# Performance work log

Hardware: AMD Instinct MI355X
Metric: run time of the kernel (lower is better)

## Reference

```python
import jax, jax.numpy as jnp
import numpy as np

N = 262144          # anchors
NUM_CLASSES = 80
DET_DIM = 4 + NUM_CLASSES
TOP_K = 1000
MAX_BOXES = 300
NMS_THRESHOLD = 0.4


def setup_inputs() -> dict:
    key = jax.random.key(0)
    k1, k2, k3, k4, k5 = jax.random.split(key, 5)
    # boxes in (x1, y1, x2, y2) format with x2 > x1, y2 > y1
    xy1 = jax.random.uniform(k1, (1, N, 2), dtype=jnp.float32) * 1000.0
    wh = jax.random.uniform(k2, (1, N, 2), dtype=jnp.float32) * 100.0 + 1.0
    boxes = jnp.concatenate([xy1, xy1 + wh], axis=-1)              # [1, N, 4]
    classification = jax.random.uniform(k3, (1, N, NUM_CLASSES), dtype=jnp.float32)
    detections = jax.random.normal(k4, (1, N, DET_DIM), dtype=jnp.float32)
    return {"boxes": boxes, "classification": classification, "detections": detections}


def _iou_matrix(b):
    # b: [K, 4] in (x1, y1, x2, y2)
    x1, y1, x2, y2 = b[:, 0], b[:, 1], b[:, 2], b[:, 3]
    area = (x2 - x1) * (y2 - y1)
    ix1 = jnp.maximum(x1[:, None], x1[None, :])
    iy1 = jnp.maximum(y1[:, None], y1[None, :])
    ix2 = jnp.minimum(x2[:, None], x2[None, :])
    iy2 = jnp.minimum(y2[:, None], y2[None, :])
    inter = jnp.maximum(ix2 - ix1, 0.0) * jnp.maximum(iy2 - iy1, 0.0)
    union = area[:, None] + area[None, :] - inter
    return inter / jnp.maximum(union, 1e-8)


def _nms(boxes, scores, iou_threshold, max_output_size):
    # Greedy NMS (tf.image.non_max_suppression semantics) on K boxes.
    K = boxes.shape[0]
    order = jnp.argsort(-scores)              # descending score
    iou = _iou_matrix(boxes[order])           # [K, K] in sorted order
    ar = jnp.arange(K)

    def body(suppressed, i):
        active = jnp.logical_not(suppressed[i])
        suppressed = suppressed | (active & (iou[i] > iou_threshold) & (ar > i))
        return suppressed, active

    _, keep = jax.lax.scan(body, jnp.zeros((K,), jnp.bool_), ar)
    # fixed-size selection of kept positions (in score order), padded with K
    sel = jnp.nonzero(keep, size=max_output_size, fill_value=K)[0]
    valid = sel < K
    order_pad = jnp.concatenate([order, jnp.zeros((1,), order.dtype)])
    return order_pad[sel], valid


def reference(boxes, classification, detections):
    b = boxes[0]                               # [N, 4]
    c = classification[0]                      # [N, C]
    d = detections[0]                          # [N, D]
    scores = jnp.max(c, axis=1)                # per-anchor best class score
    scores_k, idx_k = jax.lax.top_k(scores, TOP_K)
    b_k = b[idx_k]                             # [TOP_K, 4]
    d_k = d[idx_k]                             # [TOP_K, D]
    nms_idx, valid = _nms(b_k, scores_k, NMS_THRESHOLD, MAX_BOXES)
    # original returns a ragged [1, n_kept, D]; we return fixed [1, MAX_BOXES, D]
    # with invalid rows zeroed (padding for jit-compatibility)
    out = d_k[nms_idx] * valid[:, None].astype(d_k.dtype)
    return out[None]                           # [1, MAX_BOXES, D]
```

## Files before the change

### kernel.cpp

```cpp
#include <hip/hip_runtime.h>
#include <stdint.h>

#define N_ANCH 262144
#define NUM_CLASSES 80
#define DET_DIM 84
#define TOP_K 1000
#define MAX_BOXES 300
#define NMS_THR 0.4f

#define OFF_KEYS   0u
#define OFF_HIST1  (N_ANCH * 4u)
#define OFF_HIST2  (OFF_HIST1 + 16384u)
#define OFF_HIST3  (OFF_HIST2 + 16384u)
#define OFF_STATE  (OFF_HIST3 + 1024u)
#define OFF_LISTA  (OFF_STATE + 64u)
#define OFF_LISTB  (OFF_LISTA + 4096u)
#define OFF_TOPK   (OFF_LISTB + 16384u)
#define OFF_BOXK   (OFF_TOPK + 4096u)
#define OFF_MASK   (OFF_BOXK + 16384u)
#define OFF_SEL    (OFF_MASK + 131072u)

#define ZERO_WORDS ((16384u + 16384u + 1024u + 64u) / 4u)

__global__ __launch_bounds__(256) void k_init(uint32_t* __restrict__ z) {
    uint32_t tid = blockIdx.x * 256u + threadIdx.x;
    if (tid < ZERO_WORDS) z[tid] = 0u;
}

__global__ __launch_bounds__(256) void k_scores(const float* __restrict__ cls,
                                                uint32_t* __restrict__ keys,
                                                uint32_t* __restrict__ ghist1) {
    __shared__ uint32_t h[4096];
    for (int i = threadIdx.x; i < 4096; i += 256) h[i] = 0u;
    __syncthreads();
    int q = threadIdx.x & 3;
    int stride = gridDim.x * 64;
    for (int a = blockIdx.x * 64 + (threadIdx.x >> 2); a < N_ANCH; a += stride) {
        const float4* p = (const float4*)(cls + (size_t)a * NUM_CLASSES) + q;
        float m = -1.0f;
#pragma unroll
        for (int t = 0; t < 5; ++t) {
            float4 v = p[4 * t];
            m = fmaxf(m, fmaxf(fmaxf(v.x, v.y), fmaxf(v.z, v.w)));
        }
        m = fmaxf(m, __shfl_xor(m, 1));
        m = fmaxf(m, __shfl_xor(m, 2));
        if (q == 0) {
            uint32_t key = __float_as_uint(m);
            keys[a] = key;
            atomicAdd(&h[key >> 20], 1u);
        }
    }
    __syncthreads();
    for (int i = threadIdx.x; i < 4096; i += 256) {
        uint32_t v = h[i];
        if (v) atomicAdd(&ghist1[i], v);
    }
}

__device__ __forceinline__ void wave_scan_hist(const uint32_t* __restrict__ hist,
                                               int nbins, uint32_t k,
                                               uint32_t* __restrict__ out, int lane) {
    int per = nbins >> 6;
    int base = lane * per;
    uint32_t partial = 0;
    for (int b = 0; b < per; ++b) partial += hist[base + b];
    uint32_t si = partial;
#pragma unroll
    for (int off = 1; off < 64; off <<= 1) {
        uint32_t v = __shfl_down(si, off);
        if (lane + off < 64) si += v;
    }
    uint32_t se = si - partial;
    if (se < k && k <= si) {
        uint32_t running = se;
        for (int b = base + per - 1; b >= base; --b) {
            uint32_t hv = hist[b];
            running += hv;
            if (running >= k) {
                out[0] = (uint32_t)b;
                out[1] = k - (running - hv);
                break;
            }
        }
    }
}

__global__ __launch_bounds__(256) void k_pass2(const uint32_t* __restrict__ keys,
                                               const uint32_t* __restrict__ ghist1,
                                               uint32_t* __restrict__ ghist2,
                                               uint32_t* __restrict__ state) {
    __shared__ uint32_t sd[2];
    __shared__ uint32_t h[4096];
    if (threadIdx.x < 64) wave_scan_hist(ghist1, 4096, TOP_K, sd, threadIdx.x);
    for (int i = threadIdx.x; i < 4096; i += 256) h[i] = 0u;
    __syncthreads();
    uint32_t d1 = sd[0], k1 = sd[1];
    if (threadIdx.x == 0 && blockIdx.x == 0) { state[0] = d1; state[1] = k1; }
    int stride = gridDim.x * 256;
    for (int a = blockIdx.x * 256 + threadIdx.x; a < N_ANCH; a += stride) {
        uint32_t key = keys[a];
        if ((key >> 20) == d1) atomicAdd(&h[(key >> 8) & 0xFFFu], 1u);
    }
    __syncthreads();
    for (int i = threadIdx.x; i < 4096; i += 256) {
        uint32_t v = h[i];
        if (v) atomicAdd(&ghist2[i], v);
    }
}

__global__ __launch_bounds__(256) void k_pass3(const uint32_t* __restrict__ keys,
                                               const uint32_t* __restrict__ ghist2,
                                               uint32_t* __restrict__ ghist3,
                                               uint32_t* __restrict__ state) {
    __shared__ uint32_t sd[2];
    if (threadIdx.x < 64) {
        uint32_t k1 = state[1];
        wave_scan_hist(ghist2, 4096, k1, sd, threadIdx.x);
    }
    __syncthreads();
    uint32_t pre24 = (state[0] << 12) | sd[0];
    uint32_t k2 = sd[1];
    if (threadIdx.x == 0 && blockIdx.x == 0) { state[2] = pre24; state[3] = k2; }
    int stride = gridDim.x * 256;
    for (int a = blockIdx.x * 256 + threadIdx.x; a < N_ANCH; a += stride) {
        uint32_t key = keys[a];
        if ((key >> 8) == pre24) atomicAdd(&ghist3[key & 0xFFu], 1u);
    }
}

__global__ __launch_bounds__(256) void k_compact(const uint32_t* __restrict__ keys,
                                                 const uint32_t* __restrict__ ghist3,
                                                 uint32_t* __restrict__ state,
                                                 uint32_t* __restrict__ listA,
                                                 uint32_t* __restrict__ listB) {
    __shared__ uint32_t sd[2];
    if (threadIdx.x < 64) {
        uint32_t k2 = state[3];
        wave_scan_hist(ghist3, 256, k2, sd, threadIdx.x);
    }
    __syncthreads();
    uint32_t T = (state[2] << 8) | sd[0];
    if (threadIdx.x == 0 && blockIdx.x == 0) { state[4] = T; state[5] = sd[1]; }
    int stride = gridDim.x * 256;
    for (int a = blockIdx.x * 256 + threadIdx.x; a < N_ANCH; a += stride) {
        uint32_t key = keys[a];
        if (key > T) {
            uint32_t p = atomicAdd(&state[6], 1u);
            if (p < 1024u) listA[p] = (uint32_t)a;
        } else if (key == T) {
            uint32_t p = atomicAdd(&state[7], 1u);
            if (p < 4096u) listB[p] = (uint32_t)a;
        }
    }
}

__global__ __launch_bounds__(256) void k_rank(const uint32_t* __restrict__ keys,
                                              const uint32_t* __restrict__ state,
                                              const uint32_t* __restrict__ listA,
                                              const uint32_t* __restrict__ listB,
                                              uint32_t* __restrict__ topk) {
    __shared__ uint32_t kA[1024];
    __shared__ uint32_t iA[1024];
    uint32_t cntA = state[6]; if (cntA > 999u) cntA = 999u;
    uint32_t cntB = state[7]; if (cntB > 4096u) cntB = 4096u;
    uint32_t r = TOP_K - cntA;
    for (int i = threadIdx.x; i < (int)cntA; i += 256) {
        uint32_t idx = listA[i];
        iA[i] = idx;
        kA[i] = keys[idx];
    }
    __syncthreads();
    int t = blockIdx.x * 256 + threadIdx.x;
    if (t < (int)cntA) {
        uint32_t myk = kA[t], myi = iA[t];
        uint32_t rank = 0;
        for (uint32_t j = 0; j < cntA; ++j) {
            uint32_t kj = kA[j];
            rank += (kj > myk) || (kj == myk && iA[j] < myi);
        }
        topk[rank] = myi;
    }
    if (t < (int)cntB) {
        uint32_t myi = listB[t];
        uint32_t rank = 0;
        for (uint32_t j = 0; j < cntB; ++j)
            rank += (listB[j] < myi);
        if (rank < r) topk[cntA + rank] = myi;
    }
}

__global__ __launch_bounds__(256) void k_mask(const uint32_t* __restrict__ topk,
                                              const float4* __restrict__ boxes,
                                              unsigned long long* __restrict__ mask) {
    __shared__ float4 bx[1000];
    for (int i = threadIdx.x; i < 1000; i += 256) bx[i] = boxes[topk[i]];
    __syncthreads();
    int i = blockIdx.x;
    if (i >= 1000) {
        if (threadIdx.x < 16) mask[(size_t)i * 16 + threadIdx.x] = 0ull;
        return;
    }
    float4 bi = bx[i];
    float areai = __fmul_rn(__fsub_rn(bi.z, bi.x), __fsub_rn(bi.w, bi.y));
    int lane = threadIdx.x & 63;
    int wave = threadIdx.x >> 6;
#pragma unroll
    for (int rr = 0; rr < 4; ++rr) {
        int j = rr * 256 + threadIdx.x;
        bool bit = false;
        if (j < 1000 && j > i) {
            float4 bj = bx[j];
            float areaj = __fmul_rn(__fsub_rn(bj.z, bj.x), __fsub_rn(bj.w, bj.y));
            float ix1 = fmaxf(bi.x, bj.x);
            float iy1 = fmaxf(bi.y, bj.y);
            float ix2 = fminf(bi.z, bj.z);
            float iy2 = fminf(bi.w, bj.w);
            float iw = fmaxf(__fsub_rn(ix2, ix1), 0.0f);
            float ih = fmaxf(__fsub_rn(iy2, iy1), 0.0f);
            float inter = __fmul_rn(iw, ih);
            float uni = __fsub_rn(__fadd_rn(areai, areaj), inter);
            float den = fmaxf(uni, 1e-8f);
            float iou = inter / den;
            bit = iou > NMS_THR;
        }
        unsigned long long bal = __ballot(bit);
        if (lane == 0) mask[(size_t)i * 16 + (rr * 4 + wave)] = bal;
    }
}

__global__ __launch_bounds__(64) void k_nms(const unsigned long long* __restrict__ mask,
                                            const uint32_t* __restrict__ topk,
                                            uint32_t* __restrict__ sel) {
    __shared__ uint32_t keptList[384];
    int lane = threadIdx.x;
    uint32_t keptCount = 0;
    for (int c = 0; c < 16; ++c) {
        unsigned long long acc = 0ull;
        for (uint32_t s = (uint32_t)lane; s < keptCount; s += 64u)
            acc |= mask[(size_t)keptList[s] * 16 + c];
#pragma unroll
        for (int off = 1; off < 64; off <<= 1) acc |= __shfl_xor(acc, off);
        unsigned long long supp = acc;
        unsigned long long row = mask[(size_t)(c * 64 + lane) * 16 + c];
        for (int i = 0; i < 64; ++i) {
            unsigned long long ri = __shfl(row, i);
            if (!((supp >> i) & 1ull)) supp |= ri;
        }
        unsigned long long validm = (c == 15) ? ((1ull << 40) - 1ull) : ~0ull;
        unsigned long long kept = (~supp) & validm;
        uint32_t cnt = (uint32_t)__popcll(kept);
        if ((kept >> lane) & 1ull) {
            uint32_t pos = keptCount + (uint32_t)__popcll(kept & ((1ull << lane) - 1ull));
            if (pos < 384u) keptList[pos] = (uint32_t)(c * 64 + lane);
        }
        keptCount += cnt;
        __syncthreads();
        if (keptCount >= MAX_BOXES) break;
    }
    for (uint32_t m = (uint32_t)lane; m < MAX_BOXES; m += 64u)
        sel[m] = (m < keptCount) ? topk[keptList[m]] : 0xFFFFFFFFu;
}

__global__ __launch_bounds__(256) void k_out(const uint32_t* __restrict__ sel,
                                             const float* __restrict__ det,
                                             float* __restrict__ out) {
    int tid = blockIdx.x * 256 + threadIdx.x;
    if (tid >= MAX_BOXES * DET_DIM) return;
    int m = tid / DET_DIM;
    int e = tid - m * DET_DIM;
    uint32_t s = sel[m];
    out[tid] = (s == 0xFFFFFFFFu) ? 0.0f : det[(size_t)s * DET_DIM + e];
}

extern "C" void kernel_launch(void* const* d_in, const int* in_sizes, int n_in,
                              void* d_out, int out_size, void* d_ws, size_t ws_size,
                              hipStream_t stream) {
    const float* boxes = (const float*)d_in[0];
    const float* cls   = (const float*)d_in[1];
    const float* det   = (const float*)d_in[2];
    float* out = (float*)d_out;
    char* ws = (char*)d_ws;

    uint32_t* keys  = (uint32_t*)(ws + OFF_KEYS);
    uint32_t* h1    = (uint32_t*)(ws + OFF_HIST1);
    uint32_t* h2    = (uint32_t*)(ws + OFF_HIST2);
    uint32_t* h3    = (uint32_t*)(ws + OFF_HIST3);
    uint32_t* st    = (uint32_t*)(ws + OFF_STATE);
    uint32_t* listA = (uint32_t*)(ws + OFF_LISTA);
    uint32_t* listB = (uint32_t*)(ws + OFF_LISTB);
    uint32_t* topk  = (uint32_t*)(ws + OFF_TOPK);
    unsigned long long* mask = (unsigned long long*)(ws + OFF_MASK);
    uint32_t* sel   = (uint32_t*)(ws + OFF_SEL);

    k_init<<<dim3((ZERO_WORDS + 255) / 256), dim3(256), 0, stream>>>(h1);
    k_scores<<<dim3(512), dim3(256), 0, stream>>>(cls, keys, h1);
    k_pass2<<<dim3(256), dim3(256), 0, stream>>>(keys, h1, h2, st);
    k_pass3<<<dim3(256), dim3(256), 0, stream>>>(keys, h2, h3, st);
    k_compact<<<dim3(256), dim3(256), 0, stream>>>(keys, h3, st, listA, listB);
    k_rank<<<dim3(16), dim3(256), 0, stream>>>(keys, st, listA, listB, topk);
    k_mask<<<dim3(1024), dim3(256), 0, stream>>>(topk, (const float4*)boxes, mask);
    k_nms<<<dim3(1), dim3(64), 0, stream>>>(mask, topk, sel);
    k_out<<<dim3((MAX_BOXES * DET_DIM + 255) / 256), dim3(256), 0, stream>>>(sel, det, out);
}
```

Baseline: 248.8 us.

## Drop third radix pass and fuse rank, NMS and gather into one block

```diff
diff --git a/kernel.cpp b/kernel.cpp
--- a/kernel.cpp
+++ b/kernel.cpp
@@ -11,16 +11,11 @@
 #define OFF_KEYS   0u
 #define OFF_HIST1  (N_ANCH * 4u)
 #define OFF_HIST2  (OFF_HIST1 + 16384u)
-#define OFF_HIST3  (OFF_HIST2 + 16384u)
-#define OFF_STATE  (OFF_HIST3 + 1024u)
+#define OFF_STATE  (OFF_HIST2 + 16384u)
 #define OFF_LISTA  (OFF_STATE + 64u)
-#define OFF_LISTB  (OFF_LISTA + 4096u)
-#define OFF_TOPK   (OFF_LISTB + 16384u)
-#define OFF_BOXK   (OFF_TOPK + 4096u)
-#define OFF_MASK   (OFF_BOXK + 16384u)
-#define OFF_SEL    (OFF_MASK + 131072u)
-
-#define ZERO_WORDS ((16384u + 16384u + 1024u + 64u) / 4u)
+#define OFF_LISTC  (OFF_LISTA + 4096u)
+
+#define ZERO_WORDS ((16384u + 16384u + 64u) / 4u)
 
 __global__ __launch_bounds__(256) void k_init(uint32_t* __restrict__ z) {
     uint32_t tid = blockIdx.x * 256u + threadIdx.x;
@@ -88,15 +83,13 @@
 
 __global__ __launch_bounds__(256) void k_pass2(const uint32_t* __restrict__ keys,
                                                const uint32_t* __restrict__ ghist1,
-                                               uint32_t* __restrict__ ghist2,
-                                               uint32_t* __restrict__ state) {
+                                               uint32_t* __restrict__ ghist2) {
     __shared__ uint32_t sd[2];
     __shared__ uint32_t h[4096];
     if (threadIdx.x < 64) wave_scan_hist(ghist1, 4096, TOP_K, sd, threadIdx.x);
     for (int i = threadIdx.x; i < 4096; i += 256) h[i] = 0u;
     __syncthreads();
-    uint32_t d1 = sd[0], k1 = sd[1];
-    if (threadIdx.x == 0 && blockIdx.x == 0) { state[0] = d1; state[1] = k1; }
+    uint32_t d1 = sd[0];
     int stride = gridDim.x * 256;
     for (int a = blockIdx.x * 256 + threadIdx.x; a < N_ANCH; a += stride) {
         uint32_t key = keys[a];
@@ -109,168 +102,161 @@
     }
 }
 
-__global__ __launch_bounds__(256) void k_pass3(const uint32_t* __restrict__ keys,
-                                               const uint32_t* __restrict__ ghist2,
-                                               uint32_t* __restrict__ ghist3,
-                                               uint32_t* __restrict__ state) {
+__global__ __launch_bounds__(256) void k_compact(const uint32_t* __restrict__ keys,
+                                                 const uint32_t* __restrict__ ghist1,
+                                                 const uint32_t* __restrict__ ghist2,
+                                                 uint32_t* __restrict__ state,
+                                                 uint32_t* __restrict__ listA,
+                                                 uint32_t* __restrict__ listC) {
     __shared__ uint32_t sd[2];
-    if (threadIdx.x < 64) {
-        uint32_t k1 = state[1];
-        wave_scan_hist(ghist2, 4096, k1, sd, threadIdx.x);
-    }
-    __syncthreads();
-    uint32_t pre24 = (state[0] << 12) | sd[0];
-    uint32_t k2 = sd[1];
-    if (threadIdx.x == 0 && blockIdx.x == 0) { state[2] = pre24; state[3] = k2; }
+    __shared__ uint32_t sd2[2];
+    if (threadIdx.x < 64) wave_scan_hist(ghist1, 4096, TOP_K, sd, threadIdx.x);
+    __syncthreads();
+    uint32_t d1 = sd[0], k1 = sd[1];
+    if (threadIdx.x < 64) wave_scan_hist(ghist2, 4096, k1, sd2, threadIdx.x);
+    __syncthreads();
+    uint32_t pre24 = (d1 << 12) | sd2[0];
     int stride = gridDim.x * 256;
     for (int a = blockIdx.x * 256 + threadIdx.x; a < N_ANCH; a += stride) {
-        uint32_t key = keys[a];
-        if ((key >> 8) == pre24) atomicAdd(&ghist3[key & 0xFFu], 1u);
-    }
-}
-
-__global__ __launch_bounds__(256) void k_compact(const uint32_t* __restrict__ keys,
-                                                 const uint32_t* __restrict__ ghist3,
-                                                 uint32_t* __restrict__ state,
-                                                 uint32_t* __restrict__ listA,
-                                                 uint32_t* __restrict__ listB) {
-    __shared__ uint32_t sd[2];
-    if (threadIdx.x < 64) {
-        uint32_t k2 = state[3];
-        wave_scan_hist(ghist3, 256, k2, sd, threadIdx.x);
-    }
-    __syncthreads();
-    uint32_t T = (state[2] << 8) | sd[0];
-    if (threadIdx.x == 0 && blockIdx.x == 0) { state[4] = T; state[5] = sd[1]; }
-    int stride = gridDim.x * 256;
-    for (int a = blockIdx.x * 256 + threadIdx.x; a < N_ANCH; a += stride) {
-        uint32_t key = keys[a];
-        if (key > T) {
+        uint32_t hi = keys[a] >> 8;
+        if (hi > pre24) {
             uint32_t p = atomicAdd(&state[6], 1u);
             if (p < 1024u) listA[p] = (uint32_t)a;
-        } else if (key == T) {
+        } else if (hi == pre24) {
             uint32_t p = atomicAdd(&state[7], 1u);
-            if (p < 4096u) listB[p] = (uint32_t)a;
-        }
-    }
-}
-
-__global__ __launch_bounds__(256) void k_rank(const uint32_t* __restrict__ keys,
-                                              const uint32_t* __restrict__ state,
-                                              const uint32_t* __restrict__ listA,
-                                              const uint32_t* __restrict__ listB,
-                                              uint32_t* __restrict__ topk) {
-    __shared__ uint32_t kA[1024];
-    __shared__ uint32_t iA[1024];
-    uint32_t cntA = state[6]; if (cntA > 999u) cntA = 999u;
-    uint32_t cntB = state[7]; if (cntB > 4096u) cntB = 4096u;
+            if (p < 4096u) listC[p] = (uint32_t)a;
+        }
+    }
+}
+
+__device__ __forceinline__ bool iou_gt(float4 bi, float areai, float4 bj) {
+    float areaj = __fmul_rn(__fsub_rn(bj.z, bj.x), __fsub_rn(bj.w, bj.y));
+    float ix1 = fmaxf(bi.x, bj.x);
+    float iy1 = fmaxf(bi.y, bj.y);
+    float ix2 = fminf(bi.z, bj.z);
+    float iy2 = fminf(bi.w, bj.w);
+    float iw = fmaxf(__fsub_rn(ix2, ix1), 0.0f);
+    float ih = fmaxf(__fsub_rn(iy2, iy1), 0.0f);
+    float inter = __fmul_rn(iw, ih);
+    float uni = __fsub_rn(__fadd_rn(areai, areaj), inter);
+    float den = fmaxf(uni, 1e-8f);
+    float iou = inter / den;
+    return iou > NMS_THR;
+}
+
+__global__ __launch_bounds__(1024) void k_final(const uint32_t* __restrict__ keys,
+                                                const uint32_t* __restrict__ state,
+                                                const uint32_t* __restrict__ listA,
+                                                const uint32_t* __restrict__ listC,
+                                                const float4* __restrict__ boxes,
+                                                const float* __restrict__ det,
+                                                float* __restrict__ out) {
+    __shared__ float4 bx[1000];
+    __shared__ uint32_t tk[1000];
+    __shared__ uint32_t kA[1024], iA[1024];
+    __shared__ uint32_t kC[1024], iC[1024];
+    __shared__ unsigned long long sRow[64];
+    __shared__ unsigned long long sAcc[16];
+    __shared__ unsigned long long sSupp;
+    __shared__ uint32_t keptList[384];
+    __shared__ uint32_t sKept;
+    int t = threadIdx.x;
+
+    uint32_t cntA = state[6]; if (cntA > 999u)  cntA = 999u;
+    uint32_t cntC = state[7]; if (cntC > 1024u) cntC = 1024u;
     uint32_t r = TOP_K - cntA;
-    for (int i = threadIdx.x; i < (int)cntA; i += 256) {
-        uint32_t idx = listA[i];
-        iA[i] = idx;
-        kA[i] = keys[idx];
-    }
-    __syncthreads();
-    int t = blockIdx.x * 256 + threadIdx.x;
+
+    if (t < 1000) tk[t] = 0u;
+    if (t < (int)cntA) { uint32_t idx = listA[t]; iA[t] = idx; kA[t] = keys[idx]; }
+    if (t < (int)cntC) { uint32_t idx = listC[t]; iC[t] = idx; kC[t] = keys[idx]; }
+    __syncthreads();
+
     if (t < (int)cntA) {
-        uint32_t myk = kA[t], myi = iA[t];
-        uint32_t rank = 0;
+        uint32_t myk = kA[t], myi = iA[t], rank = 0;
         for (uint32_t j = 0; j < cntA; ++j) {
             uint32_t kj = kA[j];
             rank += (kj > myk) || (kj == myk && iA[j] < myi);
         }
-        topk[rank] = myi;
-    }
-    if (t < (int)cntB) {
-        uint32_t myi = listB[t];
-        uint32_t rank = 0;
-        for (uint32_t j = 0; j < cntB; ++j)
-            rank += (listB[j] < myi);
-        if (rank < r) topk[cntA + rank] = myi;
-    }
-}
-
-__global__ __launch_bounds__(256) void k_mask(const uint32_t* __restrict__ topk,
-                                              const float4* __restrict__ boxes,
-                                              unsigned long long* __restrict__ mask) {
-    __shared__ float4 bx[1000];
-    for (int i = threadIdx.x; i < 1000; i += 256) bx[i] = boxes[topk[i]];
-    __syncthreads();
-    int i = blockIdx.x;
-    if (i >= 1000) {
-        if (threadIdx.x < 16) mask[(size_t)i * 16 + threadIdx.x] = 0ull;
-        return;
-    }
-    float4 bi = bx[i];
-    float areai = __fmul_rn(__fsub_rn(bi.z, bi.x), __fsub_rn(bi.w, bi.y));
-    int lane = threadIdx.x & 63;
-    int wave = threadIdx.x >> 6;
-#pragma unroll
-    for (int rr = 0; rr < 4; ++rr) {
-        int j = rr * 256 + threadIdx.x;
-        bool bit = false;
-        if (j < 1000 && j > i) {
-            float4 bj = bx[j];
-            float areaj = __fmul_rn(__fsub_rn(bj.z, bj.x), __fsub_rn(bj.w, bj.y));
-            float ix1 = fmaxf(bi.x, bj.x);
-            float iy1 = fmaxf(bi.y, bj.y);
-            float ix2 = fminf(bi.z, bj.z);
-            float iy2 = fminf(bi.w, bj.w);
-            float iw = fmaxf(__fsub_rn(ix2, ix1), 0.0f);
-            float ih = fmaxf(__fsub_rn(iy2, iy1), 0.0f);
-            float inter = __fmul_rn(iw, ih);
-            float uni = __fsub_rn(__fadd_rn(areai, areaj), inter);
-            float den = fmaxf(uni, 1e-8f);
-            float iou = inter / den;
-            bit = iou > NMS_THR;
-        }
-        unsigned long long bal = __ballot(bit);
-        if (lane == 0) mask[(size_t)i * 16 + (rr * 4 + wave)] = bal;
-    }
-}
-
-__global__ __launch_bounds__(64) void k_nms(const unsigned long long* __restrict__ mask,
-                                            const uint32_t* __restrict__ topk,
-                                            uint32_t* __restrict__ sel) {
-    __shared__ uint32_t keptList[384];
-    int lane = threadIdx.x;
-    uint32_t keptCount = 0;
+        tk[rank] = myi;
+    }
+    if (t < (int)cntC) {
+        uint32_t myk = kC[t], myi = iC[t], rank = 0;
+        for (uint32_t j = 0; j < cntC; ++j) {
+            uint32_t kj = kC[j];
+            rank += (kj > myk) || (kj == myk && iC[j] < myi);
+        }
+        if (rank < r) tk[cntA + rank] = myi;
+    }
+    __syncthreads();
+    if (t < 1000) bx[t] = boxes[tk[t]];
+    __syncthreads();
+
+    int lane = t & 63;
+    int wv = t >> 6;
+    uint32_t kc = 0;
     for (int c = 0; c < 16; ++c) {
-        unsigned long long acc = 0ull;
-        for (uint32_t s = (uint32_t)lane; s < keptCount; s += 64u)
-            acc |= mask[(size_t)keptList[s] * 16 + c];
-#pragma unroll
-        for (int off = 1; off < 64; off <<= 1) acc |= __shfl_xor(acc, off);
-        unsigned long long supp = acc;
-        unsigned long long row = mask[(size_t)(c * 64 + lane) * 16 + c];
-        for (int i = 0; i < 64; ++i) {
-            unsigned long long ri = __shfl(row, i);
-            if (!((supp >> i) & 1ull)) supp |= ri;
-        }
-        unsigned long long validm = (c == 15) ? ((1ull << 40) - 1ull) : ~0ull;
-        unsigned long long kept = (~supp) & validm;
-        uint32_t cnt = (uint32_t)__popcll(kept);
-        if ((kept >> lane) & 1ull) {
-            uint32_t pos = keptCount + (uint32_t)__popcll(kept & ((1ull << lane) - 1ull));
-            if (pos < 384u) keptList[pos] = (uint32_t)(c * 64 + lane);
-        }
-        keptCount += cnt;
-        __syncthreads();
-        if (keptCount >= MAX_BOXES) break;
-    }
-    for (uint32_t m = (uint32_t)lane; m < MAX_BOXES; m += 64u)
-        sel[m] = (m < keptCount) ? topk[keptList[m]] : 0xFFFFFFFFu;
-}
-
-__global__ __launch_bounds__(256) void k_out(const uint32_t* __restrict__ sel,
-                                             const float* __restrict__ det,
-                                             float* __restrict__ out) {
-    int tid = blockIdx.x * 256 + threadIdx.x;
-    if (tid >= MAX_BOXES * DET_DIM) return;
-    int m = tid / DET_DIM;
-    int e = tid - m * DET_DIM;
-    uint32_t s = sel[m];
-    out[tid] = (s == 0xFFFFFFFFu) ? 0.0f : det[(size_t)s * DET_DIM + e];
+        int base = c * 64;
+        int chunkN = (c == 15) ? 40 : 64;
+        bool hit = false;
+        if (lane < chunkN) {
+            float4 bj = bx[base + lane];
+            for (uint32_t s = (uint32_t)wv; s < kc; s += 16u) {
+                float4 bi = bx[keptList[s]];
+                float areai = __fmul_rn(__fsub_rn(bi.z, bi.x), __fsub_rn(bi.w, bi.y));
+                hit = hit || iou_gt(bi, areai, bj);
+            }
+        }
+        unsigned long long bal = __ballot(hit);
+        if (lane == 0) sAcc[wv] = bal;
+        for (int j = wv; j < 64; j += 16) {
+            bool b = false;
+            if (j < chunkN && lane < chunkN && lane > j) {
+                float4 bi = bx[base + j];
+                float areai = __fmul_rn(__fsub_rn(bi.z, bi.x), __fsub_rn(bi.w, bi.y));
+                b = iou_gt(bi, areai, bx[base + lane]);
+            }
+            unsigned long long rb = __ballot(b);
+            if (lane == 0) sRow[j] = rb;
+        }
+        __syncthreads();
+        if (t == 0) {
+            unsigned long long acc = 0ull;
+            for (int w = 0; w < 16; ++w) acc |= sAcc[w];
+            sSupp = acc;
+        }
+        __syncthreads();
+        if (wv == 0) {
+            unsigned long long supp = sSupp;
+            unsigned long long row = sRow[lane];
+            for (int i = 0; i < 64; ++i) {
+                unsigned long long ri = __shfl(row, i);
+                if (!((supp >> i) & 1ull)) supp |= ri;
+            }
+            unsigned long long validm = (chunkN == 64) ? ~0ull : ((1ull << chunkN) - 1ull);
+            unsigned long long kept = (~supp) & validm;
+            uint32_t cnt = (uint32_t)__popcll(kept);
+            if ((kept >> lane) & 1ull) {
+                uint32_t pos = kc + (uint32_t)__popcll(kept & ((1ull << lane) - 1ull));
+                if (pos < 384u) keptList[pos] = (uint32_t)(base + lane);
+            }
+            if (lane == 0) sKept = kc + cnt;
+        }
+        __syncthreads();
+        kc = sKept;
+        __syncthreads();
+        if (kc >= MAX_BOXES) break;
+    }
+
+    for (int g = t; g < MAX_BOXES * DET_DIM; g += 1024) {
+        int m = g / DET_DIM;
+        int e = g - m * DET_DIM;
+        float v = 0.0f;
+        if ((uint32_t)m < kc) {
+            uint32_t idx = tk[keptList[m]];
+            v = det[(size_t)idx * DET_DIM + e];
+        }
+        out[g] = v;
+    }
 }
 
 extern "C" void kernel_launch(void* const* d_in, const int* in_sizes, int n_in,
@@ -285,21 +271,14 @@
     uint32_t* keys  = (uint32_t*)(ws + OFF_KEYS);
     uint32_t* h1    = (uint32_t*)(ws + OFF_HIST1);
     uint32_t* h2    = (uint32_t*)(ws + OFF_HIST2);
-    uint32_t* h3    = (uint32_t*)(ws + OFF_HIST3);
     uint32_t* st    = (uint32_t*)(ws + OFF_STATE);
     uint32_t* listA = (uint32_t*)(ws + OFF_LISTA);
-    uint32_t* listB = (uint32_t*)(ws + OFF_LISTB);
-    uint32_t* topk  = (uint32_t*)(ws + OFF_TOPK);
-    unsigned long long* mask = (unsigned long long*)(ws + OFF_MASK);
-    uint32_t* sel   = (uint32_t*)(ws + OFF_SEL);
+    uint32_t* listC = (uint32_t*)(ws + OFF_LISTC);
 
     k_init<<<dim3((ZERO_WORDS + 255) / 256), dim3(256), 0, stream>>>(h1);
     k_scores<<<dim3(512), dim3(256), 0, stream>>>(cls, keys, h1);
-    k_pass2<<<dim3(256), dim3(256), 0, stream>>>(keys, h1, h2, st);
-    k_pass3<<<dim3(256), dim3(256), 0, stream>>>(keys, h2, h3, st);
-    k_compact<<<dim3(256), dim3(256), 0, stream>>>(keys, h3, st, listA, listB);
-    k_rank<<<dim3(16), dim3(256), 0, stream>>>(keys, st, listA, listB, topk);
-    k_mask<<<dim3(1024), dim3(256), 0, stream>>>(topk, (const float4*)boxes, mask);
-    k_nms<<<dim3(1), dim3(64), 0, stream>>>(mask, topk, sel);
-    k_out<<<dim3((MAX_BOXES * DET_DIM + 255) / 256), dim3(256), 0, stream>>>(sel, det, out);
-}
+    k_pass2<<<dim3(256), dim3(256), 0, stream>>>(keys, h1, h2);
+    k_compact<<<dim3(256), dim3(256), 0, stream>>>(keys, h1, h2, st, listA, listC);
+    k_final<<<dim3(1), dim3(1024), 0, stream>>>(keys, st, listA, listC,
+                                                (const float4*)boxes, det, out);
+}
```

Result: slower. 285.5 us (+14.8%).
